# Kernel tuning notes

Measured on AMD Instinct MI355X. Metric: run time of the kernel, lower is better.

The kernel has to match this reference:

```python
import jax, jax.numpy as jnp
import numpy as np

TOP_K = 30
NUM_RBF = 16
MAX_REL = 32          # max_relative_feature
EDGE_FEATURES = 128
NUM_POS_EMB = 16
EDGE_INS = NUM_POS_EMB + NUM_RBF * 25  # 416
ONEHOT_DIM = 2 * MAX_REL + 2           # 66

# 25 (A, B) atom-pair indices into stacked order [Ca, N, C, O, Cb]
PAIR_A = np.array([0,1,2,3,4, 0,0,0,0, 1,1,1, 4,4, 3, 1,2,3,4, 2,3,4, 2,3, 2])
PAIR_B = np.array([0,1,2,3,4, 1,2,3,4, 2,3,4, 2,3, 2, 0,0,0,0, 1,1,1, 4,4, 3])


def setup_inputs() -> dict:
    key = jax.random.key(0)
    k1, k2, k3, k4, k5 = jax.random.split(key, 5)
    B, L = 4, 2048
    X = jax.random.normal(k1, (B, L, 4, 3), dtype=jnp.float32)
    mask = jnp.ones((B, L), dtype=jnp.float32)
    residue_idx = jnp.arange(B * L, dtype=jnp.int64 if jax.config.jax_enable_x64 else jnp.int32).reshape(B, L)
    # parameters
    W_pos = jax.random.normal(k2, (ONEHOT_DIM, NUM_POS_EMB), dtype=jnp.float32) * 0.02
    b_pos = jnp.zeros((NUM_POS_EMB,), dtype=jnp.float32)
    W_edge = jax.random.normal(k3, (EDGE_INS, EDGE_FEATURES), dtype=jnp.float32) * 0.02
    ln_gamma = jnp.ones((EDGE_FEATURES,), dtype=jnp.float32)
    ln_beta = jnp.zeros((EDGE_FEATURES,), dtype=jnp.float32)
    return {"X": X, "mask": mask, "residue_idx": residue_idx,
            "W_pos": W_pos, "b_pos": b_pos, "W_edge": W_edge,
            "ln_gamma": ln_gamma, "ln_beta": ln_beta}


def reference(X, mask, residue_idx, W_pos, b_pos, W_edge, ln_gamma, ln_beta):
    eps = 1e-6
    Bsz, L = X.shape[0], X.shape[1]
    K = min(TOP_K, L)

    # virtual Cb construction
    b = X[:, :, 1, :] - X[:, :, 0, :]
    c = X[:, :, 2, :] - X[:, :, 1, :]
    a = jnp.cross(b, c)
    Cb = -0.58273431 * a + 0.56802827 * b - 0.54067466 * c + X[:, :, 1, :]
    Ca = X[:, :, 1, :]
    N_ = X[:, :, 0, :]
    C_ = X[:, :, 2, :]
    O_ = X[:, :, 3, :]

    # --- _dist on Ca: masked pairwise distance + top-k smallest ---
    mask2d = mask[:, None, :] * mask[:, :, None]              # [B, L, L]
    dX = Ca[:, :, None, :] - Ca[:, None, :, :]                # [B, L, L, 3]
    D = mask2d * jnp.sqrt(jnp.sum(dX * dX, axis=-1) + eps)    # [B, L, L]
    D_max = jnp.max(D, axis=-1, keepdims=True)
    D_adjust = D + (1.0 - mask2d) * D_max
    neg_vals, E_idx = jax.lax.top_k(-D_adjust, K)             # smallest-k, ascending

    # --- 25 atom-pair distances, gathered only at neighbor indices ---
    atoms = jnp.stack([Ca, N_, C_, O_, Cb], axis=0)           # [5, B, L, 3]
    A_all = atoms[PAIR_A]                                     # [25, B, L, 3]
    B_all = atoms[PAIR_B]                                     # [25, B, L, 3]
    # gather neighbor coords: [25, B, L, K, 3]
    gather_b = jax.vmap(lambda coords, idx: coords[idx], in_axes=(0, 0))      # over batch
    gather_pb = jax.vmap(gather_b, in_axes=(0, None))                         # over pairs
    B_nb = gather_pb(B_all, E_idx)
    diff = A_all[:, :, :, None, :] - B_nb
    D_nb = jnp.sqrt(jnp.sum(diff * diff, axis=-1) + 1e-6)     # [25, B, L, K]

    # --- RBF featurization ---
    D_mu = jnp.linspace(2.0, 22.0, NUM_RBF, dtype=D_nb.dtype)
    D_sigma = (22.0 - 2.0) / NUM_RBF
    RBF = jnp.exp(-(((D_nb[..., None] - D_mu) / D_sigma) ** 2))  # [25, B, L, K, R]
    # concat order: [B, L, K, 25*R]
    RBF_all = jnp.transpose(RBF, (1, 2, 3, 0, 4)).reshape(Bsz, L, K, 25 * NUM_RBF)

    # --- relative positional encodings ---
    offset = residue_idx[:, :, None] - residue_idx[:, None, :]    # [B, L, L]
    off_nb = jnp.take_along_axis(offset, E_idx, axis=2)           # [B, L, K]
    d = jnp.clip(off_nb + MAX_REL, 0, 2 * MAX_REL)
    d_onehot = jax.nn.one_hot(d, ONEHOT_DIM, dtype=W_pos.dtype)   # [B, L, K, 66]
    E_pos = d_onehot @ W_pos + b_pos                              # [B, L, K, 16]

    # --- edge embedding + layernorm ---
    E = jnp.concatenate([E_pos, RBF_all], axis=-1)                # [B, L, K, 416]
    E = E @ W_edge                                                # [B, L, K, 128]
    mu = jnp.mean(E, axis=-1, keepdims=True)
    var = jnp.mean((E - mu) ** 2, axis=-1, keepdims=True)
    E = (E - mu) / jnp.sqrt(var + 1e-5) * ln_gamma + ln_beta
    return E
```

## Files before the change

kernel.cpp:

```cpp
#include <hip/hip_runtime.h>
#include <hip/hip_bf16.h>
#include <math.h>

#define BB      4
#define LL      2048
#define KNB     30
#define NRES    (BB*LL)
#define NEDGE   (NRES*KNB)
#define EDGE_IN 416
#define KT      13
#define ME      64
#define AST3    168
#define FINF    3.4e38f
#define LOG2E   1.44269504088896340736f

typedef __attribute__((ext_vector_type(8))) _Float16 half8;
typedef __attribute__((ext_vector_type(4))) float floatx4;

__device__ __constant__ int d_PA[25] = {0,1,2,3,4,0,0,0,0,1,1,1,4,4,3,1,2,3,4,2,3,4,2,3,2};
__device__ __constant__ int d_PB[25] = {0,1,2,3,4,1,2,3,4,2,3,4,2,3,2,0,0,0,0,1,1,1,4,4,3};

__device__ __forceinline__ unsigned short f2h_bits(float x) {
    _Float16 h = (_Float16)x;
    union { _Float16 h; unsigned short u; } v; v.h = h;
    return v.u;
}
__device__ __forceinline__ unsigned pack2h(float a, float b) {
    return (unsigned)f2h_bits(a) | ((unsigned)f2h_bits(b) << 16);
}

__global__ __launch_bounds__(256) void atoms_kernel(const float* __restrict__ X,
                                                    float* __restrict__ atoms,
                                                    float* __restrict__ caTx,
                                                    float* __restrict__ caTy,
                                                    float* __restrict__ caTz) {
    int r = blockIdx.x * blockDim.x + threadIdx.x;
    if (r >= NRES) return;
    const float* xr = X + (size_t)r * 12;
    float Nx = xr[0],  Ny = xr[1],  Nz = xr[2];
    float Ax = xr[3],  Ay = xr[4],  Az = xr[5];
    float Cx = xr[6],  Cy = xr[7],  Cz = xr[8];
    float Ox = xr[9],  Oy = xr[10], Oz = xr[11];
    float bx = Ax - Nx, by = Ay - Ny, bz = Az - Nz;
    float cx = Cx - Ax, cy = Cy - Ay, cz = Cz - Az;
    float ax = by * cz - bz * cy;
    float ay = bz * cx - bx * cz;
    float az = bx * cy - by * cx;
    float Cbx = -0.58273431f * ax + 0.56802827f * bx - 0.54067466f * cx + Ax;
    float Cby = -0.58273431f * ay + 0.56802827f * by - 0.54067466f * cy + Ay;
    float Cbz = -0.58273431f * az + 0.56802827f * bz - 0.54067466f * cz + Az;
    float* o = atoms + (size_t)r * 15;
    o[0]  = Ax;  o[1]  = Ay;  o[2]  = Az;
    o[3]  = Nx;  o[4]  = Ny;  o[5]  = Nz;
    o[6]  = Cx;  o[7]  = Cy;  o[8]  = Cz;
    o[9]  = Ox;  o[10] = Oy;  o[11] = Oz;
    o[12] = Cbx; o[13] = Cby; o[14] = Cbz;
    caTx[r] = Ax; caTy[r] = Ay; caTz[r] = Az;
}

__global__ __launch_bounds__(256, 6) void topk_kernel(const float* __restrict__ caTx,
                                                      const float* __restrict__ caTy,
                                                      const float* __restrict__ caTz,
                                                      const float* __restrict__ mask,
                                                      int* __restrict__ E_idx) {
#pragma clang fp contract(off)
    int t    = threadIdx.x;
    int wid  = t >> 6;
    int lane = t & 63;
    int bi   = blockIdx.x * 4 + wid;
    int b    = bi >> 11;
    int j0   = b << 11;

    float cx = caTx[bi], cy = caTy[bi], cz = caTz[bi];
    float mi = mask[bi];

    float aa[32];
    float lmax = 0.0f;
#pragma unroll
    for (int i = 0; i < 32; i++) {
        int j = j0 + i * 64 + lane;
        float dx = cx - caTx[j], dy = cy - caTy[j], dz = cz - caTz[j];
        float ssq = ((dx * dx + dy * dy) + dz * dz) + 1e-6f;
        float m2  = mask[j] * mi;
        float Dj  = m2 * sqrtf(ssq);
        aa[i] = Dj;
        lmax = fmaxf(lmax, Dj);
    }
    for (int off = 32; off; off >>= 1) lmax = fmaxf(lmax, __shfl_xor(lmax, off));

    float l0 = FINF, l1 = FINF, l2 = FINF, l3 = FINF;
    int   i0 = 0,    i1 = 0,    i2 = 0,    i3 = 0;
#pragma unroll
    for (int i = 0; i < 32; i++) {
        float m2 = mask[j0 + i * 64 + lane] * mi;
        float v  = aa[i] + (1.0f - m2) * lmax;
        aa[i] = v;
        bool c0 = v < l0, c1 = v < l1, c2 = v < l2, c3 = v < l3;
        l3 = c2 ? l2 : (c3 ? v : l3);  i3 = c2 ? i2 : (c3 ? i : i3);
        l2 = c1 ? l1 : (c2 ? v : l2);  i2 = c1 ? i1 : (c2 ? i : i2);
        l1 = c0 ? l0 : (c1 ? v : l1);  i1 = c0 ? i0 : (c1 ? i : i1);
        l0 = c0 ? v  : l0;             i0 = c0 ? i  : i0;
    }

    unsigned consumed = 0;
    int* outp = E_idx + (size_t)bi * KNB;
#pragma unroll 1
    for (int r = 0; r < KNB; r++) {
        float bv = l0;
        int   bj = (i0 << 6) | lane;
        for (int off = 1; off < 64; off <<= 1) {
            float ov = __shfl_xor(bv, off);
            int   oj = __shfl_xor(bj, off);
            if (ov < bv || (ov == bv && oj < bj)) { bv = ov; bj = oj; }
        }
        if (lane == 0) outp[r] = bj;
        bool mine = ((bj & 63) == lane);
        if (mine) {
            consumed |= 1u << ((unsigned)bj >> 6);
            l0 = l1; i0 = i1;
            l1 = l2; i1 = i2;
            l2 = l3; i2 = i3;
            l3 = FINF;
        }
        bool need = mine && (l0 == FINF) && (r < KNB - 1);
        if (need) {
            l0 = FINF; l1 = FINF; l2 = FINF; l3 = FINF;
            i0 = 0; i1 = 0; i2 = 0; i3 = 0;
#pragma unroll
            for (int i = 0; i < 32; i++) {
                float v = (consumed & (1u << i)) ? FINF : aa[i];
                bool c0 = v < l0, c1 = v < l1, c2 = v < l2, c3 = v < l3;
                l3 = c2 ? l2 : (c3 ? v : l3);  i3 = c2 ? i2 : (c3 ? i : i3);
                l2 = c1 ? l1 : (c2 ? v : l2);  i2 = c1 ? i1 : (c2 ? i : i2);
                l1 = c0 ? l0 : (c1 ? v : l1);  i1 = c0 ? i0 : (c1 ? i : i1);
                l0 = c0 ? v  : l0;             i0 = c0 ? i  : i0;
            }
        }
    }
}

__global__ __launch_bounds__(256) void wprep_kernel(const float* __restrict__ W_edge,
                                                    half8* __restrict__ Wfh,
                                                    half8* __restrict__ Wfl) {
    int t = blockIdx.x * blockDim.x + threadIdx.x;
    if (t >= KT * 8 * 64) return;
    int kk   = t >> 9;
    int rem  = t & 511;
    int nt   = rem >> 6;
    int lane = rem & 63;
    int n  = nt * 16 + (lane & 15);
    int kb = kk * 32 + (lane >> 4) * 8;
    half8 vh, vl;
#pragma unroll
    for (int j = 0; j < 8; j++) {
        float w = W_edge[(size_t)(kb + j) * 128 + n];
        _Float16 wh = (_Float16)w;
        vh[j] = wh;
        vl[j] = (_Float16)(w - (float)wh);
    }
    Wfh[t] = vh;
    Wfl[t] = vl;
}

__global__ __launch_bounds__(256) void edge_kernel(const float* __restrict__ atoms,
                                                   const int* __restrict__ E_idx,
                                                   const int* __restrict__ resi,
                                                   const float* __restrict__ W_pos,
                                                   const float* __restrict__ b_pos,
                                                   const half8* __restrict__ Wfh,
                                                   const half8* __restrict__ Wfl,
                                                   const float* __restrict__ gamma,
                                                   const float* __restrict__ beta,
                                                   float* __restrict__ out) {
    __shared__ _Float16 Ah[ME * AST3];
    __shared__ _Float16 Al[ME * AST3];
    __shared__ float Dl[ME][26];
    __shared__ float redS[2][ME];
    __shared__ int   s_gi[ME], s_gj[ME], s_d[ME];

    int t  = threadIdx.x;
    int e0 = blockIdx.x * ME;

    if (t < ME) {
        int e  = e0 + t;
        int gi = e / KNB;
        int k  = e - gi * KNB;
        int b  = gi >> 11;
        int j  = E_idx[(size_t)gi * KNB + k];
        s_gi[t] = gi;
        s_gj[t] = (b << 11) + j;
        int off = resi[gi] - resi[(b << 11) + j];
        int d = off + 32;
        s_d[t] = d < 0 ? 0 : (d > 64 ? 64 : d);
    }
    __syncthreads();

    for (int idx = t; idx < ME * 25; idx += 256) {
        int e = idx / 25, p = idx - e * 25;
        const float* Ar = atoms + (size_t)s_gi[e] * 15 + d_PA[p] * 3;
        const float* Br = atoms + (size_t)s_gj[e] * 15 + d_PB[p] * 3;
        float dx = Ar[0] - Br[0];
        float dy = Ar[1] - Br[1];
        float dz = Ar[2] - Br[2];
        Dl[e][p] = sqrtf(dx * dx + dy * dy + dz * dz + 1e-6f);
    }
    __syncthreads();

    int fe  = t >> 2;
    int fj4 = t & 3;
    const float* dle = Dl[fe];
    _Float16* fah = &Ah[fe * AST3];
    _Float16* fal = &Al[fe * AST3];

    {
        {
            int c = fj4 * 4;
            int dpos = s_d[fe];
            const float* wp = W_pos + dpos * 16 + c;
            float v[4];
#pragma unroll
            for (int q = 0; q < 4; q++) v[q] = wp[q] + b_pos[c + q];
            float h0 = (float)(_Float16)v[0], h1 = (float)(_Float16)v[1];
            float h2 = (float)(_Float16)v[2], h3 = (float)(_Float16)v[3];
            *(unsigned*)&fah[c + 0] = pack2h(v[0], v[1]);
            *(unsigned*)&fah[c + 2] = pack2h(v[2], v[3]);
            *(unsigned*)&fal[c + 0] = pack2h(v[0] - h0, v[1] - h1);
            *(unsigned*)&fal[c + 2] = pack2h(v[2] - h2, v[3] - h3);
        }
#pragma unroll
        for (int i = 0; i < 18; i++) {
            int c2 = 2 * (fj4 + 4 * i);
            int p  = c2 >> 4;
            int r  = c2 & 15;
            float D = dle[p];
            float mu0 = 2.0f + (float)r * (20.0f / 15.0f);
            float mu1 = 2.0f + (float)(r + 1) * (20.0f / 15.0f);
            float t0 = (D - mu0) * 0.8f;
            float t1 = (D - mu1) * 0.8f;
            float g0 = __builtin_amdgcn_exp2f(-(t0 * t0) * LOG2E);
            float g1 = __builtin_amdgcn_exp2f(-(t1 * t1) * LOG2E);
            float h0 = (float)(_Float16)g0, h1 = (float)(_Float16)g1;
            *(unsigned*)&fah[16 + c2] = pack2h(g0, g1);
            *(unsigned*)&fal[16 + c2] = pack2h(g0 - h0, g1 - h1);
        }
    }
    __syncthreads();

    int lane  = t & 63;
    int w     = t >> 6;
    int ms    = w & 1;
    int h     = w >> 1;
    int m     = lane & 15;
    int quad  = lane >> 4;
    const _Float16* pah = &Ah[(ms * 32 + m) * AST3 + quad * 8];
    const _Float16* pal = &Al[(ms * 32 + m) * AST3 + quad * 8];

    floatx4 acc[2][4];
#pragma unroll
    for (int s = 0; s < 2; s++)
#pragma unroll
        for (int c = 0; c < 4; c++) acc[s][c] = (floatx4){0.f, 0.f, 0.f, 0.f};

    half8 bh[4], bl[4], bnh[4], bnl[4];
#pragma unroll
    for (int c = 0; c < 4; c++) {
        int idx = (h * 4 + c) * 64 + lane;
        bh[c] = Wfh[idx];
        bl[c] = Wfl[idx];
    }

#pragma unroll 1
    for (int kk = 0; kk < 5; kk++) {
        half8 a_hi0 = *(const half8*)(pah + kk * 32);
        half8 a_lo0 = *(const half8*)(pal + kk * 32);
        half8 a_hi1 = *(const half8*)(pah + 16 * AST3 + kk * 32);
        half8 a_lo1 = *(const half8*)(pal + 16 * AST3 + kk * 32);
#pragma unroll
        for (int c = 0; c < 4; c++) {
            int idx = ((kk + 1) * 8 + h * 4 + c) * 64 + lane;
            bnh[c] = Wfh[idx];
            bnl[c] = Wfl[idx];
        }
#pragma unroll
        for (int c = 0; c < 4; c++) {
            acc[0][c] = __builtin_amdgcn_mfma_f32_16x16x32_f16(a_hi0, bh[c], acc[0][c], 0, 0, 0);
            acc[1][c] = __builtin_amdgcn_mfma_f32_16x16x32_f16(a_hi1, bh[c], acc[1][c], 0, 0, 0);
            acc[0][c] = __builtin_amdgcn_mfma_f32_16x16x32_f16(a_lo0, bh[c], acc[0][c], 0, 0, 0);
            acc[1][c] = __builtin_amdgcn_mfma_f32_16x16x32_f16(a_lo1, bh[c], acc[1][c], 0, 0, 0);
            acc[0][c] = __builtin_amdgcn_mfma_f32_16x16x32_f16(a_hi0, bl[c], acc[0][c], 0, 0, 0);
            acc[1][c] = __builtin_amdgcn_mfma_f32_16x16x32_f16(a_hi1, bl[c], acc[1][c], 0, 0, 0);
        }
#pragma unroll
        for (int c = 0; c < 4; c++) { bh[c] = bnh[c]; bl[c] = bnl[c]; }
    }

    __syncthreads();

    {
#pragma unroll
        for (int i = 18; i < 34; i++) {
            int c2 = 2 * (fj4 + 4 * i);
            int p  = c2 >> 4;
            int r  = c2 & 15;
            float D = dle[p];
            float mu0 = 2.0f + (float)r * (20.0f / 15.0f);
            float mu1 = 2.0f + (float)(r + 1) * (20.0f / 15.0f);
            float t0 = (D - mu0) * 0.8f;
            float t1 = (D - mu1) * 0.8f;
            float g0 = __builtin_amdgcn_exp2f(-(t0 * t0) * LOG2E);
            float g1 = __builtin_amdgcn_exp2f(-(t1 * t1) * LOG2E);
            float h0 = (float)(_Float16)g0, h1 = (float)(_Float16)g1;
            int col = c2 - 144;
            *(unsigned*)&fah[col] = pack2h(g0, g1);
            *(unsigned*)&fal[col] = pack2h(g0 - h0, g1 - h1);
        }
    }
    __syncthreads();

#pragma unroll 1
    for (int kk = 5; kk < 9; kk++) {
        half8 a_hi0 = *(const half8*)(pah + (kk - 5) * 32);
        half8 a_lo0 = *(const half8*)(pal + (kk - 5) * 32);
        half8 a_hi1 = *(const half8*)(pah + 16 * AST3 + (kk - 5) * 32);
        half8 a_lo1 = *(const half8*)(pal + 16 * AST3 + (kk - 5) * 32);
#pragma unroll
        for (int c = 0; c < 4; c++) {
            int idx = ((kk + 1) * 8 + h * 4 + c) * 64 + lane;
            bnh[c] = Wfh[idx];
            bnl[c] = Wfl[idx];
        }
#pragma unroll
        for (int c = 0; c < 4; c++) {
            acc[0][c] = __builtin_amdgcn_mfma_f32_16x16x32_f16(a_hi0, bh[c], acc[0][c], 0, 0, 0);
            acc[1][c] = __builtin_amdgcn_mfma_f32_16x16x32_f16(a_hi1, bh[c], acc[1][c], 0, 0, 0);
            acc[0][c] = __builtin_amdgcn_mfma_f32_16x16x32_f16(a_lo0, bh[c], acc[0][c], 0, 0, 0);
            acc[1][c] = __builtin_amdgcn_mfma_f32_16x16x32_f16(a_lo1, bh[c], acc[1][c], 0, 0, 0);
            acc[0][c] = __builtin_amdgcn_mfma_f32_16x16x32_f16(a_hi0, bl[c], acc[0][c], 0, 0, 0);
            acc[1][c] = __builtin_amdgcn_mfma_f32_16x16x32_f16(a_hi1, bl[c], acc[1][c], 0, 0, 0);
        }
#pragma unroll
        for (int c = 0; c < 4; c++) { bh[c] = bnh[c]; bl[c] = bnl[c]; }
    }

    __syncthreads();

    {
#pragma unroll
        for (int i = 34; i < 50; i++) {
            int c2 = 2 * (fj4 + 4 * i);
            int p  = c2 >> 4;
            int r  = c2 & 15;
            float D = dle[p];
            float mu0 = 2.0f + (float)r * (20.0f / 15.0f);
            float mu1 = 2.0f + (float)(r + 1) * (20.0f / 15.0f);
            float t0 = (D - mu0) * 0.8f;
            float t1 = (D - mu1) * 0.8f;
            float g0 = __builtin_amdgcn_exp2f(-(t0 * t0) * LOG2E);
            float g1 = __builtin_amdgcn_exp2f(-(t1 * t1) * LOG2E);
            float h0 = (float)(_Float16)g0, h1 = (float)(_Float16)g1;
            int col = c2 - 272;
            *(unsigned*)&fah[col] = pack2h(g0, g1);
            *(unsigned*)&fal[col] = pack2h(g0 - h0, g1 - h1);
        }
    }
    __syncthreads();

#pragma unroll 1
    for (int kk = 9; kk < KT; kk++) {
        half8 a_hi0 = *(const half8*)(pah + (kk - 9) * 32);
        half8 a_lo0 = *(const half8*)(pal + (kk - 9) * 32);
        half8 a_hi1 = *(const half8*)(pah + 16 * AST3 + (kk - 9) * 32);
        half8 a_lo1 = *(const half8*)(pal + 16 * AST3 + (kk - 9) * 32);
        if (kk < KT - 1) {
#pragma unroll
            for (int c = 0; c < 4; c++) {
                int idx = ((kk + 1) * 8 + h * 4 + c) * 64 + lane;
                bnh[c] = Wfh[idx];
                bnl[c] = Wfl[idx];
            }
        }
#pragma unroll
        for (int c = 0; c < 4; c++) {
            acc[0][c] = __builtin_amdgcn_mfma_f32_16x16x32_f16(a_hi0, bh[c], acc[0][c], 0, 0, 0);
            acc[1][c] = __builtin_amdgcn_mfma_f32_16x16x32_f16(a_hi1, bh[c], acc[1][c], 0, 0, 0);
            acc[0][c] = __builtin_amdgcn_mfma_f32_16x16x32_f16(a_lo0, bh[c], acc[0][c], 0, 0, 0);
            acc[1][c] = __builtin_amdgcn_mfma_f32_16x16x32_f16(a_lo1, bh[c], acc[1][c], 0, 0, 0);
            acc[0][c] = __builtin_amdgcn_mfma_f32_16x16x32_f16(a_hi0, bl[c], acc[0][c], 0, 0, 0);
            acc[1][c] = __builtin_amdgcn_mfma_f32_16x16x32_f16(a_hi1, bl[c], acc[1][c], 0, 0, 0);
        }
#pragma unroll
        for (int c = 0; c < 4; c++) { bh[c] = bnh[c]; bl[c] = bnl[c]; }
    }

#pragma unroll
    for (int s = 0; s < 2; s++) {
        int elb = ms * 32 + s * 16 + quad * 4;
        float sarr[4];
#pragma unroll
        for (int r = 0; r < 4; r++) {
            float sm = acc[s][0][r] + acc[s][1][r] + acc[s][2][r] + acc[s][3][r];
            for (int msk = 1; msk <= 8; msk <<= 1) sm += __shfl_xor(sm, msk);
            sarr[r] = sm;
        }
        if (m == 0) {
#pragma unroll
            for (int r = 0; r < 4; r++) redS[h][elb + r] = sarr[r];
        }
        __syncthreads();
        float mu[4];
#pragma unroll
        for (int r = 0; r < 4; r++) mu[r] = (redS[0][elb + r] + redS[1][elb + r]) * (1.0f / 128.0f);
        __syncthreads();
        float dvv[4][4];
#pragma unroll
        for (int r = 0; r < 4; r++) {
            float v = 0.f;
#pragma unroll
            for (int c = 0; c < 4; c++) { dvv[c][r] = acc[s][c][r] - mu[r]; v += dvv[c][r] * dvv[c][r]; }
            for (int msk = 1; msk <= 8; msk <<= 1) v += __shfl_xor(v, msk);
            if (m == 0) redS[h][elb + r] = v;
        }
        __syncthreads();
#pragma unroll
        for (int r = 0; r < 4; r++) {
            float var  = (redS[0][elb + r] + redS[1][elb + r]) * (1.0f / 128.0f);
            float rstd = rsqrtf(var + 1e-5f);
            int e = e0 + elb + r;
            float* orow = out + (size_t)e * 128;
#pragma unroll
            for (int c = 0; c < 4; c++) {
                int n = (h * 4 + c) * 16 + m;
                orow[n] = dvv[c][r] * rstd * gamma[n] + beta[n];
            }
        }
        if (s == 0) __syncthreads();
    }
}

extern "C" void kernel_launch(void* const* d_in, const int* in_sizes, int n_in,
                              void* d_out, int out_size, void* d_ws, size_t ws_size,
                              hipStream_t stream) {
    const float* X      = (const float*)d_in[0];
    const float* mask   = (const float*)d_in[1];
    const int*   resi   = (const int*)  d_in[2];
    const float* W_pos  = (const float*)d_in[3];
    const float* b_pos  = (const float*)d_in[4];
    const float* W_edge = (const float*)d_in[5];
    const float* gamma  = (const float*)d_in[6];
    const float* beta   = (const float*)d_in[7];
    float* out = (float*)d_out;

    float* atoms = (float*)d_ws;
    int*   E_idx = (int*)((char*)d_ws + (size_t)NRES * 15 * 4);
    half8* Wfh   = (half8*)((char*)d_ws + 1474560);
    half8* Wfl   = (half8*)((char*)d_ws + 1581056);
    float* caTx  = (float*)((char*)d_ws + 1687552);
    float* caTy  = (float*)((char*)d_ws + 1720320);
    float* caTz  = (float*)((char*)d_ws + 1753088);

    atoms_kernel<<<(NRES + 255) / 256, 256, 0, stream>>>(X, atoms, caTx, caTy, caTz);
    wprep_kernel<<<(KT * 8 * 64 + 255) / 256, 256, 0, stream>>>(W_edge, Wfh, Wfl);
    topk_kernel<<<NRES / 4, 256, 0, stream>>>(caTx, caTy, caTz, mask, E_idx);
    edge_kernel<<<NEDGE / ME, 256, 0, stream>>>(atoms, E_idx, resi,
                                                W_pos, b_pos, Wfh, Wfl, gamma, beta, out);
}
```

Measured before the change: 291.8 us.

## Drop activation low-half split and use two-chunk shared feature staging

Removes the fp16 low-residual part of the activation (RBF and positional features), keeping the split only for the weights. This cuts the MFMA count per k-step from 6 to 4 and halves the shared-memory staging. The freed LDS is used to stage the features in two chunks instead of three, which removes one barrier-separated phase. Activations now carry only fp16 precision, so accuracy drops somewhat.

Result: faster. 285.4 us (-2.2%).

```diff
diff --git a/kernel.cpp b/kernel.cpp
--- a/kernel.cpp
+++ b/kernel.cpp
@@ -9,8 +9,9 @@
 #define NEDGE   (NRES*KNB)
 #define EDGE_IN 416
 #define KT      13
+#define KTA     7
 #define ME      64
-#define AST3    168
+#define AST2    232
 #define FINF    3.4e38f
 #define LOG2E   1.44269504088896340736f
 
@@ -172,8 +173,7 @@
                                                    const float* __restrict__ gamma,
                                                    const float* __restrict__ beta,
                                                    float* __restrict__ out) {
-    __shared__ _Float16 Ah[ME * AST3];
-    __shared__ _Float16 Al[ME * AST3];
+    __shared__ _Float16 Ah[ME * AST2];
     __shared__ float Dl[ME][26];
     __shared__ float redS[2][ME];
     __shared__ int   s_gi[ME], s_gj[ME], s_d[ME];
@@ -209,26 +209,22 @@
     int fe  = t >> 2;
     int fj4 = t & 3;
     const float* dle = Dl[fe];
-    _Float16* fah = &Ah[fe * AST3];
-    _Float16* fal = &Al[fe * AST3];
+    _Float16* fah = &Ah[fe * AST2];
 
     {
         {
             int c = fj4 * 4;
             int dpos = s_d[fe];
             const float* wp = W_pos + dpos * 16 + c;
-            float v[4];
-#pragma unroll
-            for (int q = 0; q < 4; q++) v[q] = wp[q] + b_pos[c + q];
-            float h0 = (float)(_Float16)v[0], h1 = (float)(_Float16)v[1];
-            float h2 = (float)(_Float16)v[2], h3 = (float)(_Float16)v[3];
-            *(unsigned*)&fah[c + 0] = pack2h(v[0], v[1]);
-            *(unsigned*)&fah[c + 2] = pack2h(v[2], v[3]);
-            *(unsigned*)&fal[c + 0] = pack2h(v[0] - h0, v[1] - h1);
-            *(unsigned*)&fal[c + 2] = pack2h(v[2] - h2, v[3] - h3);
-        }
-#pragma unroll
-        for (int i = 0; i < 18; i++) {
+            float v0 = wp[0] + b_pos[c + 0];
+            float v1 = wp[1] + b_pos[c + 1];
+            float v2 = wp[2] + b_pos[c + 2];
+            float v3 = wp[3] + b_pos[c + 3];
+            *(unsigned*)&fah[c + 0] = pack2h(v0, v1);
+            *(unsigned*)&fah[c + 2] = pack2h(v2, v3);
+        }
+#pragma unroll
+        for (int i = 0; i < 26; i++) {
             int c2 = 2 * (fj4 + 4 * i);
             int p  = c2 >> 4;
             int r  = c2 & 15;
@@ -239,9 +235,7 @@
             float t1 = (D - mu1) * 0.8f;
             float g0 = __builtin_amdgcn_exp2f(-(t0 * t0) * LOG2E);
             float g1 = __builtin_amdgcn_exp2f(-(t1 * t1) * LOG2E);
-            float h0 = (float)(_Float16)g0, h1 = (float)(_Float16)g1;
             *(unsigned*)&fah[16 + c2] = pack2h(g0, g1);
-            *(unsigned*)&fal[16 + c2] = pack2h(g0 - h0, g1 - h1);
         }
     }
     __syncthreads();
@@ -252,8 +246,7 @@
     int h     = w >> 1;
     int m     = lane & 15;
     int quad  = lane >> 4;
-    const _Float16* pah = &Ah[(ms * 32 + m) * AST3 + quad * 8];
-    const _Float16* pal = &Al[(ms * 32 + m) * AST3 + quad * 8];
+    const _Float16* pah = &Ah[(ms * 32 + m) * AST2 + quad * 8];
 
     floatx4 acc[2][4];
 #pragma unroll
@@ -270,11 +263,9 @@
     }
 
 #pragma unroll 1
-    for (int kk = 0; kk < 5; kk++) {
+    for (int kk = 0; kk < KTA; kk++) {
         half8 a_hi0 = *(const half8*)(pah + kk * 32);
-        half8 a_lo0 = *(const half8*)(pal + kk * 32);
-        half8 a_hi1 = *(const half8*)(pah + 16 * AST3 + kk * 32);
-        half8 a_lo1 = *(const half8*)(pal + 16 * AST3 + kk * 32);
+        half8 a_hi1 = *(const half8*)(pah + 16 * AST2 + kk * 32);
 #pragma unroll
         for (int c = 0; c < 4; c++) {
             int idx = ((kk + 1) * 8 + h * 4 + c) * 64 + lane;
@@ -285,8 +276,6 @@
         for (int c = 0; c < 4; c++) {
             acc[0][c] = __builtin_amdgcn_mfma_f32_16x16x32_f16(a_hi0, bh[c], acc[0][c], 0, 0, 0);
             acc[1][c] = __builtin_amdgcn_mfma_f32_16x16x32_f16(a_hi1, bh[c], acc[1][c], 0, 0, 0);
-            acc[0][c] = __builtin_amdgcn_mfma_f32_16x16x32_f16(a_lo0, bh[c], acc[0][c], 0, 0, 0);
-            acc[1][c] = __builtin_amdgcn_mfma_f32_16x16x32_f16(a_lo1, bh[c], acc[1][c], 0, 0, 0);
             acc[0][c] = __builtin_amdgcn_mfma_f32_16x16x32_f16(a_hi0, bl[c], acc[0][c], 0, 0, 0);
             acc[1][c] = __builtin_amdgcn_mfma_f32_16x16x32_f16(a_hi1, bl[c], acc[1][c], 0, 0, 0);
         }
@@ -298,7 +287,7 @@
 
     {
 #pragma unroll
-        for (int i = 18; i < 34; i++) {
+        for (int i = 26; i < 50; i++) {
             int c2 = 2 * (fj4 + 4 * i);
             int p  = c2 >> 4;
             int r  = c2 & 15;
@@ -309,68 +298,16 @@
             float t1 = (D - mu1) * 0.8f;
             float g0 = __builtin_amdgcn_exp2f(-(t0 * t0) * LOG2E);
             float g1 = __builtin_amdgcn_exp2f(-(t1 * t1) * LOG2E);
-            float h0 = (float)(_Float16)g0, h1 = (float)(_Float16)g1;
-            int col = c2 - 144;
+            int col = c2 - 208;
             *(unsigned*)&fah[col] = pack2h(g0, g1);
-            *(unsigned*)&fal[col] = pack2h(g0 - h0, g1 - h1);
         }
     }
     __syncthreads();
 
 #pragma unroll 1
-    for (int kk = 5; kk < 9; kk++) {
-        half8 a_hi0 = *(const half8*)(pah + (kk - 5) * 32);
-        half8 a_lo0 = *(const half8*)(pal + (kk - 5) * 32);
-        half8 a_hi1 = *(const half8*)(pah + 16 * AST3 + (kk - 5) * 32);
-        half8 a_lo1 = *(const half8*)(pal + 16 * AST3 + (kk - 5) * 32);
-#pragma unroll
-        for (int c = 0; c < 4; c++) {
-            int idx = ((kk + 1) * 8 + h * 4 + c) * 64 + lane;
-            bnh[c] = Wfh[idx];
-            bnl[c] = Wfl[idx];
-        }
-#pragma unroll
-        for (int c = 0; c < 4; c++) {
-            acc[0][c] = __builtin_amdgcn_mfma_f32_16x16x32_f16(a_hi0, bh[c], acc[0][c], 0, 0, 0);
-            acc[1][c] = __builtin_amdgcn_mfma_f32_16x16x32_f16(a_hi1, bh[c], acc[1][c], 0, 0, 0);
-            acc[0][c] = __builtin_amdgcn_mfma_f32_16x16x32_f16(a_lo0, bh[c], acc[0][c], 0, 0, 0);
-            acc[1][c] = __builtin_amdgcn_mfma_f32_16x16x32_f16(a_lo1, bh[c], acc[1][c], 0, 0, 0);
-            acc[0][c] = __builtin_amdgcn_mfma_f32_16x16x32_f16(a_hi0, bl[c], acc[0][c], 0, 0, 0);
-            acc[1][c] = __builtin_amdgcn_mfma_f32_16x16x32_f16(a_hi1, bl[c], acc[1][c], 0, 0, 0);
-        }
-#pragma unroll
-        for (int c = 0; c < 4; c++) { bh[c] = bnh[c]; bl[c] = bnl[c]; }
-    }
-
-    __syncthreads();
-
-    {
-#pragma unroll
-        for (int i = 34; i < 50; i++) {
-            int c2 = 2 * (fj4 + 4 * i);
-            int p  = c2 >> 4;
-            int r  = c2 & 15;
-            float D = dle[p];
-            float mu0 = 2.0f + (float)r * (20.0f / 15.0f);
-            float mu1 = 2.0f + (float)(r + 1) * (20.0f / 15.0f);
-            float t0 = (D - mu0) * 0.8f;
-            float t1 = (D - mu1) * 0.8f;
-            float g0 = __builtin_amdgcn_exp2f(-(t0 * t0) * LOG2E);
-            float g1 = __builtin_amdgcn_exp2f(-(t1 * t1) * LOG2E);
-            float h0 = (float)(_Float16)g0, h1 = (float)(_Float16)g1;
-            int col = c2 - 272;
-            *(unsigned*)&fah[col] = pack2h(g0, g1);
-            *(unsigned*)&fal[col] = pack2h(g0 - h0, g1 - h1);
-        }
-    }
-    __syncthreads();
-
-#pragma unroll 1
-    for (int kk = 9; kk < KT; kk++) {
-        half8 a_hi0 = *(const half8*)(pah + (kk - 9) * 32);
-        half8 a_lo0 = *(const half8*)(pal + (kk - 9) * 32);
-        half8 a_hi1 = *(const half8*)(pah + 16 * AST3 + (kk - 9) * 32);
-        half8 a_lo1 = *(const half8*)(pal + 16 * AST3 + (kk - 9) * 32);
+    for (int kk = KTA; kk < KT; kk++) {
+        half8 a_hi0 = *(const half8*)(pah + (kk - KTA) * 32);
+        half8 a_hi1 = *(const half8*)(pah + 16 * AST2 + (kk - KTA) * 32);
         if (kk < KT - 1) {
 #pragma unroll
             for (int c = 0; c < 4; c++) {
@@ -383,8 +320,6 @@
         for (int c = 0; c < 4; c++) {
             acc[0][c] = __builtin_amdgcn_mfma_f32_16x16x32_f16(a_hi0, bh[c], acc[0][c], 0, 0, 0);
             acc[1][c] = __builtin_amdgcn_mfma_f32_16x16x32_f16(a_hi1, bh[c], acc[1][c], 0, 0, 0);
-            acc[0][c] = __builtin_amdgcn_mfma_f32_16x16x32_f16(a_lo0, bh[c], acc[0][c], 0, 0, 0);
-            acc[1][c] = __builtin_amdgcn_mfma_f32_16x16x32_f16(a_lo1, bh[c], acc[1][c], 0, 0, 0);
             acc[0][c] = __builtin_amdgcn_mfma_f32_16x16x32_f16(a_hi0, bl[c], acc[0][c], 0, 0, 0);
             acc[1][c] = __builtin_amdgcn_mfma_f32_16x16x32_f16(a_hi1, bl[c], acc[1][c], 0, 0, 0);
         }
```
